# Kernel tuning notes

Measured on AMD Instinct MI355X. Metric: run time of the kernel, lower is better.

## Reference

```python
import jax, jax.numpy as jnp
import numpy as np

N, IN_FEAT, D1, D2, NUM_CLASSES = 8192, 2048, 512, 128, 10


def setup_inputs() -> dict:
    key = jax.random.key(0)
    ks = jax.random.split(key, 12)

    def xavier(k, shape):
        fan_in, fan_out = shape[1], shape[0]
        lim = np.sqrt(6.0 / (fan_in + fan_out))
        return jax.random.uniform(k, shape, jnp.float32, -lim, lim)

    return {
        "x": jax.random.normal(ks[0], (N, 1, IN_FEAT), jnp.float32),
        "W1": xavier(ks[1], (D1, IN_FEAT)), "b1": jnp.zeros((D1,), jnp.float32),
        "W2": xavier(ks[2], (D2, D1)), "b2": jnp.zeros((D2,), jnp.float32),
        # conv1d kernel_size=1 weights, squeezed to (out, in)
        "Wq": jax.random.normal(ks[3], (D2, D2), jnp.float32) * 0.05,
        "bq": jnp.zeros((D2,), jnp.float32),
        "Wk": jax.random.normal(ks[4], (D2, D2), jnp.float32) * 0.05,
        "bk": jnp.zeros((D2,), jnp.float32),
        "gamma": jnp.ones((1,), jnp.float32),
        "W3": xavier(ks[5], (NUM_CLASSES, D2)), "b3": jnp.zeros((NUM_CLASSES,), jnp.float32),
    }


def reference(x, W1, b1, W2, b2, Wq, bq, Wk, bk, gamma, W3, b3):
    # MLP stack over patches: (N, 1, in) -> (N, 1, 128)
    h = jax.nn.relu(jnp.einsum("nbi,oi->nbo", x, W1) + b1)
    h = jax.nn.relu(jnp.einsum("nbi,oi->nbo", h, W2) + b2)
    # permute(1, 2, 0): (1, C, N)
    xp = jnp.transpose(h, (1, 2, 0))
    # 1x1 conv projections (pointwise linear over channels)
    q = jnp.einsum("oc,bcn->bno", Wq, xp) + bq            # (1, N, C)
    k = jnp.einsum("oc,bcn->bcn", Wk, xp) + bk[None, :, None]  # (1, C, N)
    energy = jnp.einsum("bnc,bcm->bnm", q, k)             # (1, N, N)
    attention = jax.nn.softmax(energy, axis=-1)
    # out = bmm(x, attention^T): (1, C, N)
    out = jnp.einsum("bcm,bnm->bcn", xp, attention)
    out = gamma * out + xp
    x2 = out.mean(axis=-1)                                 # (1, C)
    logits = x2 @ W3.T + b3                                # (1, num_classes)
    return (logits, attention)
```

## Files before the change

### kernel.cpp

```cpp
#include <hip/hip_runtime.h>
#include <hip/hip_bf16.h>

typedef __attribute__((ext_vector_type(8))) __bf16 bf16x8;
typedef __attribute__((ext_vector_type(4))) __bf16 bf16x4;
typedef __attribute__((ext_vector_type(4))) float f32x4;

#define N_TOK 8192
#define IN_FEAT 2048
#define D1 512
#define D2 128
#define QBLK 128
#define KCHUNK 1024
#define KTILE 128
#define NKC (N_TOK / KCHUNK)
#define NQB (N_TOK / QBLK)

__device__ __forceinline__ void gload_lds16(const __bf16* g, __bf16* l) {
    __builtin_amdgcn_global_load_lds(
        (const __attribute__((address_space(1))) void*)g,
        (__attribute__((address_space(3))) void*)l,
        16, 0, 0);
}

__device__ __forceinline__ void stage_tile(const __bf16* __restrict__ g,
                                           __bf16* lds, int w, int lane) {
#pragma unroll
    for (int i = 0; i < 8; ++i) {
        int row   = i * 16 + w * 4 + (lane >> 4);
        int chunk = (lane & 15) ^ (row & 7);
        gload_lds16(g + (size_t)row * 128 + chunk * 8, lds + i * 2048 + w * 512);
    }
}

__device__ __forceinline__ bf16x8 rd_frag(const __bf16* lds, int row, int chunk) {
    return *(const bf16x8*)(lds + row * 128 + ((chunk ^ (row & 7)) * 8));
}

__global__ __launch_bounds__(256)
void prep(const float* __restrict__ W1, __bf16* __restrict__ w1b,
          const float* __restrict__ W2, __bf16* __restrict__ w2b,
          const float* __restrict__ Wq, __bf16* __restrict__ wqb,
          const float* __restrict__ Wk, float* __restrict__ wksum,
          float* __restrict__ colw, float* __restrict__ xw, float* __restrict__ xh) {
    int b = blockIdx.x, t = threadIdx.x;
    const float* src = nullptr; __bf16* dst = nullptr; int i = 0;
    if (b < 1024)      { src = W1; dst = w1b; i = b * 256 + t; }
    else if (b < 1088) { src = W2; dst = w2b; i = (b - 1024) * 256 + t; }
    else if (b < 1104) { src = Wq; dst = wqb; i = (b - 1088) * 256 + t; }
    else if (b < 1136) { colw[(b - 1104) * 256 + t] = 0.0f; return; }
    else {
        if (t < D2) {
            float s = 0.0f;
            for (int o = 0; o < D2; ++o) s += Wk[o * D2 + t];
            wksum[t] = s;
            xw[t] = 0.0f; xh[t] = 0.0f;
        }
        return;
    }
    float4 v = ((const float4*)src)[i];
    bf16x4 o;
    o[0] = (__bf16)v.x; o[1] = (__bf16)v.y; o[2] = (__bf16)v.z; o[3] = (__bf16)v.w;
    ((bf16x4*)dst)[i] = o;
}

__global__ __launch_bounds__(256)
void gemm1_k(const float* __restrict__ x, const __bf16* __restrict__ w1b,
             const float* __restrict__ b1, __bf16* __restrict__ h1b) {
    __shared__ __bf16 lA[128 * 32];
    __shared__ __bf16 lB[64 * 32];

    const int t    = threadIdx.x;
    const int lane = t & 63;
    const int w    = t >> 6;
    const int wr   = w >> 1;
    const int wc   = w & 1;
    const int b    = blockIdx.x;
    const int m0   = (b & 63) * 128;
    const int n0   = (b >> 6) * 64;

    const int rS = w * 16 + (lane >> 2);
    const int cS = (lane & 3) * 8;
    const int fr = lane & 15;
    const int hi = lane >> 4;
    const int ko = hi * 8;
    const int rj = hi * 4;

    const int ar = t >> 3;
    const int ac = (t & 7) * 4;

    f32x4 acc[4][2] = {};

    float4 regs[4];
#pragma unroll
    for (int i = 0; i < 4; ++i)
        regs[i] = *(const float4*)&x[(size_t)(m0 + i * 32 + ar) * IN_FEAT + ac];

    for (int k0 = 0; k0 < IN_FEAT; k0 += 32) {
        __syncthreads();
#pragma unroll
        for (int i = 0; i < 4; ++i) {
            bf16x4 o;
            o[0] = (__bf16)regs[i].x; o[1] = (__bf16)regs[i].y;
            o[2] = (__bf16)regs[i].z; o[3] = (__bf16)regs[i].w;
            *(bf16x4*)&lA[(i * 32 + ar) * 32 + ac] = o;
        }
        gload_lds16(w1b + (size_t)(n0 + rS) * IN_FEAT + k0 + cS, lB + w * 512);
        __syncthreads();

        if (k0 + 32 < IN_FEAT) {
#pragma unroll
            for (int i = 0; i < 4; ++i)
                regs[i] = *(const float4*)&x[(size_t)(m0 + i * 32 + ar) * IN_FEAT + k0 + 32 + ac];
        }

        bf16x8 af[4], bf[2];
#pragma unroll
        for (int m = 0; m < 4; ++m)
            af[m] = *(const bf16x8*)&lA[(wr * 64 + m * 16 + fr) * 32 + ko];
#pragma unroll
        for (int n = 0; n < 2; ++n)
            bf[n] = *(const bf16x8*)&lB[(wc * 32 + n * 16 + fr) * 32 + ko];
#pragma unroll
        for (int m = 0; m < 4; ++m)
#pragma unroll
            for (int n = 0; n < 2; ++n)
                acc[m][n] = __builtin_amdgcn_mfma_f32_16x16x32_bf16(af[m], bf[n], acc[m][n], 0, 0, 0);
    }

#pragma unroll
    for (int n = 0; n < 2; ++n) {
        int col = n0 + wc * 32 + n * 16 + fr;
        float bv = b1[col];
#pragma unroll
        for (int m = 0; m < 4; ++m) {
            int row = m0 + wr * 64 + m * 16 + rj;
#pragma unroll
            for (int j = 0; j < 4; ++j)
                h1b[(size_t)(row + j) * D1 + col] = (__bf16)fmaxf(acc[m][n][j] + bv, 0.0f);
        }
    }
}

__global__ __launch_bounds__(256)
void mlp2_k(const __bf16* __restrict__ h1b, const __bf16* __restrict__ w2b,
            const float* __restrict__ b2, const __bf16* __restrict__ wqb,
            const float* __restrict__ bq, const float* __restrict__ wksum,
            const float* __restrict__ bk, __bf16* __restrict__ h2b,
            __bf16* __restrict__ kb, __bf16* __restrict__ qb) {
    __shared__ __bf16 lA[32 * 32];
    __shared__ __bf16 lB[128 * 32];
    __shared__ __bf16 lH[32 * 128];

    const int t    = threadIdx.x;
    const int lane = t & 63;
    const int w    = t >> 6;
    const int fr   = lane & 15;
    const int hi   = lane >> 4;
    const int ko   = hi * 8;
    const int m0   = blockIdx.x * 32;

    f32x4 acc[2][2] = {};

    for (int k0 = 0; k0 < D1; k0 += 32) {
        __syncthreads();
        if (w < 2)
            gload_lds16(h1b + (size_t)(m0 + w * 16 + (lane >> 2)) * D1 + k0 + (lane & 3) * 8,
                        lA + w * 512);
#pragma unroll
        for (int i = 0; i < 2; ++i) {
            int row = w * 32 + i * 16 + (lane >> 2);
            gload_lds16(w2b + (size_t)row * D1 + k0 + (lane & 3) * 8,
                        lB + w * 1024 + i * 512);
        }
        __syncthreads();

        bf16x8 af[2], bf[2];
#pragma unroll
        for (int m = 0; m < 2; ++m)
            af[m] = *(const bf16x8*)&lA[(m * 16 + fr) * 32 + ko];
#pragma unroll
        for (int n = 0; n < 2; ++n)
            bf[n] = *(const bf16x8*)&lB[(w * 32 + n * 16 + fr) * 32 + ko];
#pragma unroll
        for (int m = 0; m < 2; ++m)
#pragma unroll
            for (int n = 0; n < 2; ++n)
                acc[m][n] = __builtin_amdgcn_mfma_f32_16x16x32_bf16(af[m], bf[n], acc[m][n], 0, 0, 0);
    }

#pragma unroll
    for (int n = 0; n < 2; ++n) {
        int col = w * 32 + n * 16 + fr;
        float bv = b2[col], wv = wksum[col], bkv = bk[col];
#pragma unroll
        for (int m = 0; m < 2; ++m) {
#pragma unroll
            for (int j = 0; j < 4; ++j) {
                int row = m * 16 + hi * 4 + j;
                float v = fmaxf(acc[m][n][j] + bv, 0.0f);
                h2b[(size_t)(m0 + row) * D2 + col] = (__bf16)v;
                kb [(size_t)(m0 + row) * D2 + col] = (__bf16)(wv * v + bkv);
                lH[row * 128 + (((col >> 3) ^ (row & 7)) * 8) + (col & 7)] = (__bf16)v;
            }
        }
    }
    __syncthreads();

    f32x4 acc2[2][2] = {};
#pragma unroll
    for (int kk = 0; kk < 4; ++kk) {
        bf16x8 af2[2], bf2[2];
#pragma unroll
        for (int m = 0; m < 2; ++m) {
            int row = m * 16 + fr;
            af2[m] = *(const bf16x8*)&lH[row * 128 + (((kk * 4 + hi) ^ (row & 7)) * 8)];
        }
#pragma unroll
        for (int n = 0; n < 2; ++n)
            bf2[n] = *(const bf16x8*)&wqb[(size_t)(w * 32 + n * 16 + fr) * D2 + kk * 32 + ko];
#pragma unroll
        for (int m = 0; m < 2; ++m)
#pragma unroll
            for (int n = 0; n < 2; ++n)
                acc2[m][n] = __builtin_amdgcn_mfma_f32_16x16x32_bf16(af2[m], bf2[n], acc2[m][n], 0, 0, 0);
    }
#pragma unroll
    for (int n = 0; n < 2; ++n) {
        int col = w * 32 + n * 16 + fr;
        float bv = bq[col];
#pragma unroll
        for (int m = 0; m < 2; ++m)
#pragma unroll
            for (int j = 0; j < 4; ++j) {
                int row = m0 + m * 16 + hi * 4 + j;
                qb[(size_t)row * D2 + col] = (__bf16)(acc2[m][n][j] + bv);
            }
    }
}

template<int PASS>
__global__ __launch_bounds__(256, 2)
void fa_kernel(const __bf16* __restrict__ qbuf, const __bf16* __restrict__ kbuf,
               float* __restrict__ pm, float* __restrict__ pl,
               float* __restrict__ attn, float* __restrict__ colw)
{
    __shared__ __bf16 Kl[2][KTILE * 128];
    __shared__ float rowM_l[QBLK], rowInv_l[QBLK];

    const int t    = threadIdx.x;
    const int lane = t & 63;
    const int w    = t >> 6;
    const int wr   = w >> 1;
    const int wc   = w & 1;
    const int fr   = lane & 15;
    const int hi   = lane >> 4;
    const int ck   = blockIdx.x;
    const int q0   = blockIdx.y * QBLK;
    const int kr0  = ck * KCHUNK;

    stage_tile(qbuf + (size_t)q0 * D2, Kl[0], w, lane);
    __syncthreads();
    bf16x8 af[4][4];
#pragma unroll
    for (int m = 0; m < 4; ++m)
#pragma unroll
        for (int kk = 0; kk < 4; ++kk)
            af[m][kk] = rd_frag(Kl[0], wr * 64 + m * 16 + fr, kk * 4 + hi);

    if constexpr (PASS == 2) {
        if (t < QBLK) {
            int r = q0 + t;
            float M = -1e30f;
#pragma unroll
            for (int c = 0; c < 2 * NKC; ++c) M = fmaxf(M, pm[(size_t)c * N_TOK + r]);
            float L = 0.0f;
#pragma unroll
            for (int c = 0; c < 2 * NKC; ++c)
                L += pl[(size_t)c * N_TOK + r] * __expf(pm[(size_t)c * N_TOK + r] - M);
            rowM_l[t] = M;
            rowInv_l[t] = 1.0f / L;
        }
    }
    __syncthreads();

    float mloc[4][4], lloc[4][4], Mr[4][4], Ir[4][4];
#pragma unroll
    for (int m = 0; m < 4; ++m)
#pragma unroll
        for (int j = 0; j < 4; ++j) {
            if constexpr (PASS == 1) { mloc[m][j] = -1e30f; lloc[m][j] = 0.0f; }
            else {
                int rl = wr * 64 + m * 16 + hi * 4 + j;
                Mr[m][j] = rowM_l[rl]; Ir[m][j] = rowInv_l[rl];
            }
        }

    stage_tile(kbuf + (size_t)kr0 * D2, Kl[0], w, lane);
    __syncthreads();

    for (int kt = 0; kt < KCHUNK / KTILE; ++kt) {
        const __bf16* cur = Kl[kt & 1];
        if (kt + 1 < KCHUNK / KTILE)
            stage_tile(kbuf + (size_t)(kr0 + (kt + 1) * KTILE) * D2, Kl[(kt + 1) & 1], w, lane);

        f32x4 acc[4][4] = {};
#pragma unroll
        for (int kk = 0; kk < 4; ++kk) {
            bf16x8 bfr[4];
#pragma unroll
            for (int n = 0; n < 4; ++n)
                bfr[n] = rd_frag(cur, wc * 64 + n * 16 + fr, kk * 4 + hi);
#pragma unroll
            for (int m = 0; m < 4; ++m)
#pragma unroll
                for (int n = 0; n < 4; ++n)
                    acc[m][n] = __builtin_amdgcn_mfma_f32_16x16x32_bf16(af[m][kk], bfr[n], acc[m][n], 0, 0, 0);
        }

        if constexpr (PASS == 1) {
#pragma unroll
            for (int m = 0; m < 4; ++m)
#pragma unroll
                for (int j = 0; j < 4; ++j) {
                    float a0 = acc[m][0][j], a1 = acc[m][1][j], a2 = acc[m][2][j], a3 = acc[m][3][j];
                    float t4 = fmaxf(fmaxf(a0, a1), fmaxf(a2, a3));
                    float mo = mloc[m][j];
                    float mn = fmaxf(mo, t4);
                    float s  = __expf(a0 - mn) + __expf(a1 - mn) + __expf(a2 - mn) + __expf(a3 - mn);
                    lloc[m][j] = lloc[m][j] * __expf(mo - mn) + s;
                    mloc[m][j] = mn;
                }
        } else {
            float csum[4] = {0.0f, 0.0f, 0.0f, 0.0f};
            const int colbase = kr0 + kt * KTILE + wc * 64;
#pragma unroll
            for (int m = 0; m < 4; ++m) {
#pragma unroll
                for (int n = 0; n < 4; ++n) {
                    int col = colbase + n * 16 + fr;
#pragma unroll
                    for (int j = 0; j < 4; ++j) {
                        int row = q0 + wr * 64 + m * 16 + hi * 4 + j;
                        float p = __expf(acc[m][n][j] - Mr[m][j]) * Ir[m][j];
                        attn[(size_t)row * N_TOK + col] = p;
                        csum[n] += p;
                    }
                }
            }
#pragma unroll
            for (int n = 0; n < 4; ++n) {
                csum[n] += __shfl_xor(csum[n], 16);
                csum[n] += __shfl_xor(csum[n], 32);
            }
            if (lane < 16) {
#pragma unroll
                for (int n = 0; n < 4; ++n)
                    atomicAdd(&colw[colbase + n * 16 + lane], csum[n]);
            }
        }
        __syncthreads();
    }

    if constexpr (PASS == 1) {
        const size_t slot = (size_t)(ck * 2 + wc) * N_TOK;
#pragma unroll
        for (int m = 0; m < 4; ++m)
#pragma unroll
            for (int j = 0; j < 4; ++j) {
                float M = mloc[m][j];
#pragma unroll
                for (int off = 1; off <= 8; off <<= 1) M = fmaxf(M, __shfl_xor(M, off));
                float l = lloc[m][j] * __expf(mloc[m][j] - M);
#pragma unroll
                for (int off = 1; off <= 8; off <<= 1) l += __shfl_xor(l, off);
                if ((lane & 15) == 0) {
                    int r = q0 + wr * 64 + m * 16 + hi * 4 + j;
                    pm[slot + r] = M;
                    pl[slot + r] = l;
                }
            }
    }
}

__global__ __launch_bounds__(256)
void reduce_x2(const __bf16* __restrict__ h2b, const float* __restrict__ colw,
               float* __restrict__ xw, float* __restrict__ xh) {
    int b = blockIdx.x, t = threadIdx.x;
    int c = t & 127, half = t >> 7;
    float aw = 0.0f, ah = 0.0f;
    for (int m = b * 128 + half; m < (b + 1) * 128; m += 2) {
        float h  = (float)h2b[(size_t)m * D2 + c];
        float wv = colw[m];
        aw += wv * h;
        ah += h;
    }
    atomicAdd(&xw[c], aw);
    atomicAdd(&xh[c], ah);
}

__global__ void logits_k(const float* __restrict__ xw, const float* __restrict__ xh,
                         const float* __restrict__ gamma, const float* __restrict__ W3,
                         const float* __restrict__ b3, float* __restrict__ out) {
    __shared__ float x2[D2];
    int t = threadIdx.x;
    float g = gamma[0];
    if (t < D2) x2[t] = (g * xw[t] + xh[t]) * (1.0f / (float)N_TOK);
    __syncthreads();
    if (t < 10) {
        float s = b3[t];
        for (int c = 0; c < D2; ++c) s += x2[c] * W3[t * D2 + c];
        out[t] = s;
    }
}

extern "C" void kernel_launch(void* const* d_in, const int* in_sizes, int n_in,
                              void* d_out, int out_size, void* d_ws, size_t ws_size,
                              hipStream_t stream) {
    const float* x     = (const float*)d_in[0];
    const float* W1    = (const float*)d_in[1];
    const float* b1    = (const float*)d_in[2];
    const float* W2    = (const float*)d_in[3];
    const float* b2    = (const float*)d_in[4];
    const float* Wq    = (const float*)d_in[5];
    const float* bq    = (const float*)d_in[6];
    const float* Wk    = (const float*)d_in[7];
    const float* bk    = (const float*)d_in[8];
    const float* gamma = (const float*)d_in[9];
    const float* W3    = (const float*)d_in[10];
    const float* b3    = (const float*)d_in[11];

    float* out  = (float*)d_out;
    float* attn = out + 10;

    char* p = (char*)d_ws;
    __bf16* w1b = (__bf16*)p; p += (size_t)D1 * IN_FEAT * 2;
    __bf16* w2b = (__bf16*)p; p += (size_t)D2 * D1 * 2;
    __bf16* wqb = (__bf16*)p; p += (size_t)D2 * D2 * 2;
    __bf16* h1b = (__bf16*)p; p += (size_t)N_TOK * D1 * 2;
    __bf16* h2b = (__bf16*)p; p += (size_t)N_TOK * D2 * 2;
    __bf16* qb  = (__bf16*)p; p += (size_t)N_TOK * D2 * 2;
    __bf16* kb  = (__bf16*)p; p += (size_t)N_TOK * D2 * 2;
    float* pm     = (float*)p; p += (size_t)2 * NKC * N_TOK * 4;
    float* pl     = (float*)p; p += (size_t)2 * NKC * N_TOK * 4;
    float* colw   = (float*)p; p += N_TOK * 4;
    float* wksum  = (float*)p; p += D2 * 4;
    float* xw     = (float*)p; p += D2 * 4;
    float* xh     = (float*)p; p += D2 * 4;

    prep<<<1137, 256, 0, stream>>>(W1, w1b, W2, w2b, Wq, wqb, Wk, wksum, colw, xw, xh);

    gemm1_k<<<512, 256, 0, stream>>>(x, w1b, b1, h1b);
    mlp2_k<<<N_TOK / 32, 256, 0, stream>>>(h1b, w2b, b2, wqb, bq, wksum, bk, h2b, kb, qb);

    fa_kernel<1><<<dim3(NKC, NQB), 256, 0, stream>>>(qb, kb, pm, pl, nullptr, nullptr);
    fa_kernel<2><<<dim3(NKC, NQB), 256, 0, stream>>>(qb, kb, pm, pl, attn, colw);

    reduce_x2<<<64, 256, 0, stream>>>(h2b, colw, xw, xh);
    logits_k<<<1, 128, 0, stream>>>(xw, xh, gamma, W3, b3, out);
}
```

Before: 292.5 us.

## Use exp2 with pre-scaled Q, lazy max rescale, and direct global K fragment loads

Q is scaled by log2(e) when it is stored, so the softmax kernels can call a raw v_exp_f32 (exp2) instead of __expf. Pass 1 now rescales the running max only when a wave sees a new value more than a threshold above the current max, which skips most rescale exps. The LDS double-buffered K/Q staging and its barriers are removed, and MFMA fragments are loaded straight from global memory through the cache. This cuts transcendental and sync overhead but gives up LDS reuse of K tiles, which may raise global and L2 traffic.

```diff
diff --git a/kernel.cpp b/kernel.cpp
--- a/kernel.cpp
+++ b/kernel.cpp
@@ -14,26 +14,19 @@
 #define KTILE 128
 #define NKC (N_TOK / KCHUNK)
 #define NQB (N_TOK / QBLK)
+#define LOG2E 1.44269504f
+
+__device__ __forceinline__ float fexp2(float x) {
+    float r;
+    asm("v_exp_f32 %0, %1" : "=v"(r) : "v"(x));
+    return r;
+}
 
 __device__ __forceinline__ void gload_lds16(const __bf16* g, __bf16* l) {
     __builtin_amdgcn_global_load_lds(
         (const __attribute__((address_space(1))) void*)g,
         (__attribute__((address_space(3))) void*)l,
         16, 0, 0);
-}
-
-__device__ __forceinline__ void stage_tile(const __bf16* __restrict__ g,
-                                           __bf16* lds, int w, int lane) {
-#pragma unroll
-    for (int i = 0; i < 8; ++i) {
-        int row   = i * 16 + w * 4 + (lane >> 4);
-        int chunk = (lane & 15) ^ (row & 7);
-        gload_lds16(g + (size_t)row * 128 + chunk * 8, lds + i * 2048 + w * 512);
-    }
-}
-
-__device__ __forceinline__ bf16x8 rd_frag(const __bf16* lds, int row, int chunk) {
-    return *(const bf16x8*)(lds + row * 128 + ((chunk ^ (row & 7)) * 8));
 }
 
 __global__ __launch_bounds__(256)
@@ -233,7 +226,7 @@
 #pragma unroll
             for (int j = 0; j < 4; ++j) {
                 int row = m0 + m * 16 + hi * 4 + j;
-                qb[(size_t)row * D2 + col] = (__bf16)(acc2[m][n][j] + bv);
+                qb[(size_t)row * D2 + col] = (__bf16)((acc2[m][n][j] + bv) * LOG2E);
             }
     }
 }
@@ -244,7 +237,6 @@
                float* __restrict__ pm, float* __restrict__ pl,
                float* __restrict__ attn, float* __restrict__ colw)
 {
-    __shared__ __bf16 Kl[2][KTILE * 128];
     __shared__ float rowM_l[QBLK], rowInv_l[QBLK];
 
     const int t    = threadIdx.x;
@@ -258,15 +250,14 @@
     const int q0   = blockIdx.y * QBLK;
     const int kr0  = ck * KCHUNK;
 
-    stage_tile(qbuf + (size_t)q0 * D2, Kl[0], w, lane);
-    __syncthreads();
     bf16x8 af[4][4];
 #pragma unroll
     for (int m = 0; m < 4; ++m)
 #pragma unroll
         for (int kk = 0; kk < 4; ++kk)
-            af[m][kk] = rd_frag(Kl[0], wr * 64 + m * 16 + fr, kk * 4 + hi);
-
+            af[m][kk] = *(const bf16x8*)&qbuf[(size_t)(q0 + wr * 64 + m * 16 + fr) * D2 + kk * 32 + hi * 8];
+
+    float mloc[4][4], lloc[4][4], Mr[4][4], Ir[4][4];
     if constexpr (PASS == 2) {
         if (t < QBLK) {
             int r = q0 + t;
@@ -276,32 +267,30 @@
             float L = 0.0f;
 #pragma unroll
             for (int c = 0; c < 2 * NKC; ++c)
-                L += pl[(size_t)c * N_TOK + r] * __expf(pm[(size_t)c * N_TOK + r] - M);
+                L += pl[(size_t)c * N_TOK + r] * fexp2(pm[(size_t)c * N_TOK + r] - M);
             rowM_l[t] = M;
             rowInv_l[t] = 1.0f / L;
         }
-    }
-    __syncthreads();
-
-    float mloc[4][4], lloc[4][4], Mr[4][4], Ir[4][4];
-#pragma unroll
-    for (int m = 0; m < 4; ++m)
-#pragma unroll
-        for (int j = 0; j < 4; ++j) {
-            if constexpr (PASS == 1) { mloc[m][j] = -1e30f; lloc[m][j] = 0.0f; }
-            else {
+        __syncthreads();
+#pragma unroll
+        for (int m = 0; m < 4; ++m)
+#pragma unroll
+            for (int j = 0; j < 4; ++j) {
                 int rl = wr * 64 + m * 16 + hi * 4 + j;
                 Mr[m][j] = rowM_l[rl]; Ir[m][j] = rowInv_l[rl];
             }
-        }
-
-    stage_tile(kbuf + (size_t)kr0 * D2, Kl[0], w, lane);
-    __syncthreads();
-
+    } else {
+#pragma unroll
+        for (int m = 0; m < 4; ++m)
+#pragma unroll
+            for (int j = 0; j < 4; ++j) { mloc[m][j] = -1e30f; lloc[m][j] = 0.0f; }
+    }
+
+    const __bf16* kbase = kbuf + (size_t)(kr0 + wc * 64 + fr) * D2 + hi * 8;
+
+#pragma unroll 1
     for (int kt = 0; kt < KCHUNK / KTILE; ++kt) {
-        const __bf16* cur = Kl[kt & 1];
-        if (kt + 1 < KCHUNK / KTILE)
-            stage_tile(kbuf + (size_t)(kr0 + (kt + 1) * KTILE) * D2, Kl[(kt + 1) & 1], w, lane);
+        const __bf16* kp = kbase + (size_t)kt * KTILE * D2;
 
         f32x4 acc[4][4] = {};
 #pragma unroll
@@ -309,7 +298,7 @@
             bf16x8 bfr[4];
 #pragma unroll
             for (int n = 0; n < 4; ++n)
-                bfr[n] = rd_frag(cur, wc * 64 + n * 16 + fr, kk * 4 + hi);
+                bfr[n] = *(const bf16x8*)&kp[(size_t)n * 16 * D2 + kk * 32];
 #pragma unroll
             for (int m = 0; m < 4; ++m)
 #pragma unroll
@@ -324,11 +313,13 @@
                 for (int j = 0; j < 4; ++j) {
                     float a0 = acc[m][0][j], a1 = acc[m][1][j], a2 = acc[m][2][j], a3 = acc[m][3][j];
                     float t4 = fmaxf(fmaxf(a0, a1), fmaxf(a2, a3));
+                    if (!__all(t4 <= mloc[m][j] + 11.5f)) {
+                        float mn = fmaxf(mloc[m][j], t4);
+                        lloc[m][j] *= fexp2(mloc[m][j] - mn);
+                        mloc[m][j] = mn;
+                    }
                     float mo = mloc[m][j];
-                    float mn = fmaxf(mo, t4);
-                    float s  = __expf(a0 - mn) + __expf(a1 - mn) + __expf(a2 - mn) + __expf(a3 - mn);
-                    lloc[m][j] = lloc[m][j] * __expf(mo - mn) + s;
-                    mloc[m][j] = mn;
+                    lloc[m][j] += fexp2(a0 - mo) + fexp2(a1 - mo) + fexp2(a2 - mo) + fexp2(a3 - mo);
                 }
         } else {
             float csum[4] = {0.0f, 0.0f, 0.0f, 0.0f};
@@ -341,7 +332,7 @@
 #pragma unroll
                     for (int j = 0; j < 4; ++j) {
                         int row = q0 + wr * 64 + m * 16 + hi * 4 + j;
-                        float p = __expf(acc[m][n][j] - Mr[m][j]) * Ir[m][j];
+                        float p = fexp2(acc[m][n][j] - Mr[m][j]) * Ir[m][j];
                         attn[(size_t)row * N_TOK + col] = p;
                         csum[n] += p;
                     }
@@ -358,7 +349,6 @@
                     atomicAdd(&colw[colbase + n * 16 + lane], csum[n]);
             }
         }
-        __syncthreads();
     }
 
     if constexpr (PASS == 1) {
@@ -370,7 +360,7 @@
                 float M = mloc[m][j];
 #pragma unroll
                 for (int off = 1; off <= 8; off <<= 1) M = fmaxf(M, __shfl_xor(M, off));
-                float l = lloc[m][j] * __expf(mloc[m][j] - M);
+                float l = lloc[m][j] * fexp2(mloc[m][j] - M);
 #pragma unroll
                 for (int off = 1; off <= 8; off <<= 1) l += __shfl_xor(l, off);
                 if ((lane & 15) == 0) {
```

After: 254.8 us. -12.9%, faster.
